# Kernel tuning notes

Measured on AMD Instinct MI355X. Metric: run time of the kernel, lower is better.

## Reference

```python
import jax, jax.numpy as jnp
import numpy as np

EPS = 1e-9
# i = 7,6,...,-1 use exp_factor = -(4**i); i = -2 uses 0.0 (matches torch's reversed(range(-2,8)))
EXP_FACTORS = np.array([-(4.0 ** i) for i in range(7, -2, -1)] + [0.0], dtype=np.float32)


def setup_inputs() -> dict:
    key = jax.random.key(0)
    k1, k2 = jax.random.split(key)
    B, N, D = 16, 2048, 3
    preds = jax.random.normal(k1, (B, N, D), dtype=jnp.float32)
    labels = jax.random.normal(k2, (B, N, D), dtype=jnp.float32)
    return {"preds": preds, "labels": labels}


def _pairwise_dist(p1, p2):
    # ||p1||^2 + ||p2||^2 - 2 p1 . p2  -> [B, N, N]
    p1n = jnp.sum(p1 * p1, axis=-1)[..., :, None]
    p2n = jnp.sum(p2 * p2, axis=-1)[..., None, :]
    return p1n + p2n - 2.0 * jnp.einsum('bnd,bmd->bnm', p1, p2)


def _approx_match(pwdist):
    B, N, _ = pwdist.shape
    match0 = jnp.zeros_like(pwdist)
    cost0 = jnp.ones((B, 1, N), dtype=pwdist.dtype)      # per-target remaining capacity
    curr0 = jnp.ones((B, N, 1), dtype=pwdist.dtype)      # per-source remaining currency

    def step(carry, ef):
        match, cost, currency = carry
        bids = jnp.exp(ef * pwdist) * cost
        bids = bids * currency / (jnp.sum(bids, axis=1, keepdims=True) + EPS)
        bid_wt = jnp.minimum(cost / (jnp.sum(bids, axis=1, keepdims=True) + EPS), 1.0)
        bids = bids * bid_wt
        match = match + bids
        cost = jnp.maximum(cost - jnp.sum(bids, axis=1, keepdims=True), 0.0)
        currency = jnp.maximum(currency - jnp.sum(bids, axis=2, keepdims=True), 0.0)
        return (match, cost, currency), None

    (match, _, _), _ = jax.lax.scan(step, (match0, cost0, curr0), jnp.asarray(EXP_FACTORS))
    return match


def reference(preds, labels):
    pwdist = _pairwise_dist(preds, labels)
    match = _approx_match(pwdist)
    return jnp.sum(match * pwdist)
```

## Files before the change

kernel.cpp:

```cpp
#include <hip/hip_runtime.h>
#include <cstddef>

#define BB    16
#define NN    2048
#define BN    (BB * NN)
#define TPB   512
#define SPLIT 16
#define TILE  128
#define MC    2
#define CHUNK 1024
#define EPSF  1e-9f

typedef float f2 __attribute__((ext_vector_type(2)));

__device__ __forceinline__ float fast_exp2(float x) {
#if __has_builtin(__builtin_amdgcn_exp2f)
    return __builtin_amdgcn_exp2f(x);
#else
    return exp2f(x);
#endif
}

__global__ void prep(const float* __restrict__ preds, const float* __restrict__ labels,
                     float4* __restrict__ Prow, float4* __restrict__ Lcol) {
    int i = blockIdx.x * 256 + threadIdx.x;
    const float* p = preds + (size_t)i * 3;
    float x = p[0], y = p[1], z = p[2];
    Prow[i] = make_float4(x, y, z, x * x + y * y + z * z);
    const float* l = labels + (size_t)i * 3;
    float a = l[0], c = l[1], d = l[2];
    Lcol[i] = make_float4(a, c, d, a * a + c * c + d * d);
}

__global__ __launch_bounds__(TPB, 4) void passA(
    const float4* __restrict__ Prow, const float4* __restrict__ Lcol,
    const float* __restrict__ curprev, float* __restrict__ curout,
    const float* __restrict__ RSp, const float* __restrict__ RRp,
    float* __restrict__ RSz, float* __restrict__ RRz,
    float* __restrict__ S, float* __restrict__ T,
    float* __restrict__ out, float c1, int k)
{
    __shared__ float s_cu[TILE];
    const int blk = blockIdx.x;
    const int split = blk & (SPLIT - 1), mc = (blk >> 4) & 1, b = blk >> 5;
    const int t = threadIdx.x;
    const int base = b * NN;
    const int row0 = split * TILE;

    if (t < TILE) {
        int idx = base + row0 + t;
        float cu, contrib = 0.f;
        if (k == 0) cu = 1.f;
        else {
            float cup = curprev[idx], rs = RSp[idx], rr = RRp[idx];
            contrib = cup * rr;
            cu = fmaxf(cup * (1.f - rs), 0.f);
        }
        s_cu[t] = cu;
        if (mc == 0) {
            curout[idx] = cu;
            RSz[idx] = 0.f; RRz[idx] = 0.f;
        }
        if (k > 0 && mc == 0) {
#pragma unroll
            for (int o = 32; o > 0; o >>= 1) contrib += __shfl_down(contrib, o, 64);
            if ((t & 63) == 0) atomicAdd(out, contrib);
        }
    }

    const int m0 = mc * CHUNK + t;
    float4 L0 = Lcol[base + m0], L1 = Lcol[base + m0 + TPB];
    const float n2c1 = -2.f * c1;
    f2 gx = (f2){n2c1 * L0.x, n2c1 * L1.x};
    f2 gy = (f2){n2c1 * L0.y, n2c1 * L1.y};
    f2 gz = (f2){n2c1 * L0.z, n2c1 * L1.z};
    f2 am = (f2){c1 * L0.w, c1 * L1.w};
    f2 Sa = (f2){0.f, 0.f}, Ta = (f2){0.f, 0.f};
    __syncthreads();

    const float4* prow = Prow + base + row0;
#pragma unroll 4
    for (int j = 0; j < TILE; j++) {
        float4 P = prow[j];
        float cu = s_cu[j];
        f2 arg = P.x * gx + (P.y * gy + (P.z * gz + (am + c1 * P.w)));
        f2 e; e.x = fast_exp2(arg.x); e.y = fast_exp2(arg.y);
        Sa += e;
        Ta += e * cu;
    }
    int i0 = base + m0, i1 = base + m0 + TPB;
    atomicAdd(&S[i0], Sa.x); atomicAdd(&S[i1], Sa.y);
    atomicAdd(&T[i0], Ta.x); atomicAdd(&T[i1], Ta.y);
}

__global__ __launch_bounds__(TPB, 4) void passB(
    const float4* __restrict__ Prow, const float4* __restrict__ Lcol,
    const float* __restrict__ S, const float* __restrict__ T,
    const float* __restrict__ costprev, float* __restrict__ costout,
    float* __restrict__ Sz, float* __restrict__ Tz,
    float* __restrict__ RS, float* __restrict__ RR,
    float c1, float invc1, int k, int last)
{
    __shared__ float s_cc[TILE];
    const int blk = blockIdx.x;
    const int split = blk & (SPLIT - 1), nc = (blk >> 4) & 1, b = blk >> 5;
    const int t = threadIdx.x;
    const int base = b * NN;
    const int col0 = split * TILE;

    if (t < TILE) {
        int idx = base + col0 + t;
        float Sv = S[idx], Tv = T[idx];
        float cost = (k == 0) ? 1.f : costprev[idx];
        float D1 = fmaf(cost, Sv, EPSF);
        float S2 = cost * Tv / D1;
        float bw = fminf(cost / (S2 + EPSF), 1.f);
        s_cc[t] = cost * bw / D1;
        if (nc == 0) {
            costout[idx] = fmaxf(fmaf(-S2, bw, cost), 0.f);
            Sz[idx] = 0.f; Tz[idx] = 0.f;
        }
    }

    const int n0 = nc * CHUNK + t;
    float4 P0 = Prow[base + n0], P1 = Prow[base + n0 + TPB];
    const float fx = last ? 1.f : -2.f * c1;
    f2 hx = (f2){fx * P0.x, fx * P1.x};
    f2 hy = (f2){fx * P0.y, fx * P1.y};
    f2 hz = (f2){fx * P0.z, fx * P1.z};
    f2 hn = last ? (f2){P0.w, P1.w} : (f2){c1 * P0.w, c1 * P1.w};
    f2 RSa = (f2){0.f, 0.f}, RRa = (f2){0.f, 0.f};
    __syncthreads();

    const float4* lcol = Lcol + base + col0;
    int i0 = base + n0, i1 = base + n0 + TPB;
    if (!last) {
#pragma unroll 4
        for (int j = 0; j < TILE; j++) {
            float4 L = lcol[j];
            float ccj = s_cc[j];
            f2 arg = L.x * hx + (L.y * hy + (L.z * hz + (hn + c1 * L.w)));
            f2 e; e.x = fast_exp2(arg.x); e.y = fast_exp2(arg.y);
            f2 w = e * ccj;
            RSa += w;
            RRa += w * arg;
        }
        atomicAdd(&RS[i0], RSa.x); atomicAdd(&RS[i1], RSa.y);
        atomicAdd(&RR[i0], RRa.x * invc1); atomicAdd(&RR[i1], RRa.y * invc1);
    } else {
#pragma unroll 4
        for (int j = 0; j < TILE; j++) {
            float4 L = lcol[j];
            float ccj = s_cc[j];
            f2 dot = L.x * hx + (L.y * hy + L.z * hz);
            f2 pw = (hn + L.w) - 2.f * dot;
            RRa += ccj * pw;
        }
        atomicAdd(&RR[i0], RRa.x); atomicAdd(&RR[i1], RRa.y);
    }
}

__global__ __launch_bounds__(TPB) void finalK(const float* __restrict__ cur,
                                              const float* __restrict__ RR,
                                              float* __restrict__ out)
{
    int i = blockIdx.x * TPB + threadIdx.x;
    float cb = cur[i] * RR[i];
#pragma unroll
    for (int o = 32; o > 0; o >>= 1) cb += __shfl_down(cb, o, 64);
    if ((threadIdx.x & 63) == 0) atomicAdd(out, cb);
}

extern "C" void kernel_launch(void* const* d_in, const int* in_sizes, int n_in,
                              void* d_out, int out_size, void* d_ws, size_t ws_size,
                              hipStream_t stream) {
    const float* preds  = (const float*)d_in[0];
    const float* labels = (const float*)d_in[1];
    float* out = (float*)d_out;
    float* ws  = (float*)d_ws;

    float* S[2]     = {ws + 0 * BN, ws + 2 * BN};
    float* T[2]     = {ws + 1 * BN, ws + 3 * BN};
    float* RS[2]    = {ws + 4 * BN, ws + 6 * BN};
    float* RR[2]    = {ws + 5 * BN, ws + 7 * BN};
    float* curb[2]  = {ws + 8 * BN, ws + 9 * BN};
    float* costb[2] = {ws + 10 * BN, ws + 11 * BN};
    float4* Prow = (float4*)(ws + 12 * BN);
    float4* Lcol = Prow + BN;

    hipMemsetAsync(d_out, 0, sizeof(float), stream);
    hipMemsetAsync(ws, 0, (size_t)2 * BN * sizeof(float), stream);
    prep<<<BN / 256, 256, 0, stream>>>(preds, labels, Prow, Lcol);

    static const float efs[10] = {-16384.0f, -4096.0f, -1024.0f, -256.0f, -64.0f,
                                  -16.0f, -4.0f, -1.0f, -0.25f, 0.0f};
    const float log2e = 1.44269504088896f;
    const int grid = BB * SPLIT * MC;
    for (int k = 0; k < 10; k++) {
        float c1 = efs[k] * log2e;
        float invc1 = (efs[k] != 0.0f) ? 1.0f / c1 : 0.0f;
        int pk = k & 1, pp = (k + 1) & 1;
        passA<<<grid, TPB, 0, stream>>>(Prow, Lcol,
            curb[pp], curb[pk],
            RS[pp], RR[pp],
            RS[pk], RR[pk],
            S[pk], T[pk],
            out, c1, k);
        passB<<<grid, TPB, 0, stream>>>(Prow, Lcol,
            S[pk], T[pk],
            costb[pk], costb[pp],
            S[pp], T[pp],
            RS[pk], RR[pk],
            c1, invc1, k, (k == 9) ? 1 : 0);
    }
    finalK<<<BN / TPB, TPB, 0, stream>>>(curb[1], RR[1], out);
}
```

Measured before the change: 376.7 us.

## Fuse all auction iterations into one persistent kernel with per-batch grid barriers

Replaces the 20 passA/passB launches plus finalK with a single persistent kernel of 256 blocks of 1024 threads. Consecutive phases are separated by spin-wait barriers that count arrivals per batch, and S/T/RS/RR are reset in place with system-scope atomics instead of double buffering. The exp-free last iteration (ef=0) is computed in closed form from per-batch reductions of cost-weighted label moments. This removes launch overhead and per-launch state reloads, at the cost of fewer blocks (less parallelism), spin-barrier latency, a risk of deadlock if not all blocks are co-resident, and staging tiles through global memory instead of LDS.

New measurement: 481.1 us. +27.7%, slower.

```diff
diff --git a/kernel.cpp b/kernel.cpp
--- a/kernel.cpp
+++ b/kernel.cpp
@@ -4,12 +4,13 @@
 #define BB    16
 #define NN    2048
 #define BN    (BB * NN)
-#define TPB   512
+#define TPB   1024
 #define SPLIT 16
 #define TILE  128
-#define MC    2
-#define CHUNK 1024
+#define GRIDB (BB * SPLIT)
 #define EPSF  1e-9f
+#define CTRPAD 64
+#define NBAR  20
 
 typedef float f2 __attribute__((ext_vector_type(2)));
 
@@ -19,6 +20,27 @@
 #else
     return exp2f(x);
 #endif
+}
+__device__ __forceinline__ float sysload(const float* p) {
+    return __hip_atomic_load(p, __ATOMIC_RELAXED, __HIP_MEMORY_SCOPE_SYSTEM);
+}
+__device__ __forceinline__ void sysstore(float* p, float v) {
+    __hip_atomic_store(p, v, __ATOMIC_RELAXED, __HIP_MEMORY_SCOPE_SYSTEM);
+}
+
+__device__ __forceinline__ void bbar(int* c) {
+    __syncthreads();
+    if (threadIdx.x == 0) {
+        __hip_atomic_fetch_add(c, 1, __ATOMIC_ACQ_REL, __HIP_MEMORY_SCOPE_SYSTEM);
+        int spins = 0;
+        while (__hip_atomic_load(c, __ATOMIC_RELAXED, __HIP_MEMORY_SCOPE_SYSTEM) < SPLIT) {
+#if __has_builtin(__builtin_amdgcn_s_sleep)
+            __builtin_amdgcn_s_sleep(8);
+#endif
+            if (++spins > (1 << 20)) break;
+        }
+    }
+    __syncthreads();
 }
 
 __global__ void prep(const float* __restrict__ preds, const float* __restrict__ labels,
@@ -32,143 +54,135 @@
     Lcol[i] = make_float4(a, c, d, a * a + c * c + d * d);
 }
 
-__global__ __launch_bounds__(TPB, 4) void passA(
+__global__ __launch_bounds__(TPB, 4) void emd_all(
     const float4* __restrict__ Prow, const float4* __restrict__ Lcol,
-    const float* __restrict__ curprev, float* __restrict__ curout,
-    const float* __restrict__ RSp, const float* __restrict__ RRp,
-    float* __restrict__ RSz, float* __restrict__ RRz,
     float* __restrict__ S, float* __restrict__ T,
-    float* __restrict__ out, float c1, int k)
+    float* __restrict__ RS, float* __restrict__ RR,
+    float* __restrict__ AUX, int* __restrict__ ctr,
+    float4* __restrict__ st4, float* __restrict__ st1,
+    float* __restrict__ out)
 {
-    __shared__ float s_cu[TILE];
-    const int blk = blockIdx.x;
-    const int split = blk & (SPLIT - 1), mc = (blk >> 4) & 1, b = blk >> 5;
+    __shared__ float s_red[2];
+    const int blk = blockIdx.x, split = blk & (SPLIT - 1), b = blk >> 4;
     const int t = threadIdx.x;
-    const int base = b * NN;
-    const int row0 = split * TILE;
-
-    if (t < TILE) {
-        int idx = base + row0 + t;
-        float cu, contrib = 0.f;
-        if (k == 0) cu = 1.f;
-        else {
-            float cup = curprev[idx], rs = RSp[idx], rr = RRp[idx];
-            contrib = cup * rr;
-            cu = fmaxf(cup * (1.f - rs), 0.f);
-        }
-        s_cu[t] = cu;
-        if (mc == 0) {
-            curout[idx] = cu;
-            RSz[idx] = 0.f; RRz[idx] = 0.f;
-        }
-        if (k > 0 && mc == 0) {
-#pragma unroll
-            for (int o = 32; o > 0; o >>= 1) contrib += __shfl_down(contrib, o, 64);
-            if ((t & 63) == 0) atomicAdd(out, contrib);
-        }
-    }
-
-    const int m0 = mc * CHUNK + t;
-    float4 L0 = Lcol[base + m0], L1 = Lcol[base + m0 + TPB];
-    const float n2c1 = -2.f * c1;
-    f2 gx = (f2){n2c1 * L0.x, n2c1 * L1.x};
-    f2 gy = (f2){n2c1 * L0.y, n2c1 * L1.y};
-    f2 gz = (f2){n2c1 * L0.z, n2c1 * L1.z};
-    f2 am = (f2){c1 * L0.w, c1 * L1.w};
-    f2 Sa = (f2){0.f, 0.f}, Ta = (f2){0.f, 0.f};
-    __syncthreads();
-
-    const float4* prow = Prow + base + row0;
-#pragma unroll 4
-    for (int j = 0; j < TILE; j++) {
-        float4 P = prow[j];
-        float cu = s_cu[j];
-        f2 arg = P.x * gx + (P.y * gy + (P.z * gz + (am + c1 * P.w)));
-        f2 e; e.x = fast_exp2(arg.x); e.y = fast_exp2(arg.y);
-        Sa += e;
-        Ta += e * cu;
-    }
-    int i0 = base + m0, i1 = base + m0 + TPB;
-    atomicAdd(&S[i0], Sa.x); atomicAdd(&S[i1], Sa.y);
-    atomicAdd(&T[i0], Ta.x); atomicAdd(&T[i1], Ta.y);
-}
-
-__global__ __launch_bounds__(TPB, 4) void passB(
-    const float4* __restrict__ Prow, const float4* __restrict__ Lcol,
-    const float* __restrict__ S, const float* __restrict__ T,
-    const float* __restrict__ costprev, float* __restrict__ costout,
-    float* __restrict__ Sz, float* __restrict__ Tz,
-    float* __restrict__ RS, float* __restrict__ RR,
-    float c1, float invc1, int k, int last)
-{
-    __shared__ float s_cc[TILE];
-    const int blk = blockIdx.x;
-    const int split = blk & (SPLIT - 1), nc = (blk >> 4) & 1, b = blk >> 5;
-    const int t = threadIdx.x;
-    const int base = b * NN;
-    const int col0 = split * TILE;
-
-    if (t < TILE) {
-        int idx = base + col0 + t;
-        float Sv = S[idx], Tv = T[idx];
-        float cost = (k == 0) ? 1.f : costprev[idx];
-        float D1 = fmaf(cost, Sv, EPSF);
-        float S2 = cost * Tv / D1;
-        float bw = fminf(cost / (S2 + EPSF), 1.f);
-        s_cc[t] = cost * bw / D1;
-        if (nc == 0) {
-            costout[idx] = fmaxf(fmaf(-S2, bw, cost), 0.f);
-            Sz[idx] = 0.f; Tz[idx] = 0.f;
-        }
-    }
-
-    const int n0 = nc * CHUNK + t;
-    float4 P0 = Prow[base + n0], P1 = Prow[base + n0 + TPB];
-    const float fx = last ? 1.f : -2.f * c1;
-    f2 hx = (f2){fx * P0.x, fx * P1.x};
-    f2 hy = (f2){fx * P0.y, fx * P1.y};
-    f2 hz = (f2){fx * P0.z, fx * P1.z};
-    f2 hn = last ? (f2){P0.w, P1.w} : (f2){c1 * P0.w, c1 * P1.w};
-    f2 RSa = (f2){0.f, 0.f}, RRa = (f2){0.f, 0.f};
-    __syncthreads();
-
-    const float4* lcol = Lcol + base + col0;
-    int i0 = base + n0, i1 = base + n0 + TPB;
-    if (!last) {
+    const int base = b * NN, i0 = base + split * TILE;
+    const int sb = blk * TILE;
+
+    float4 L0 = Lcol[base + t], L1 = Lcol[base + t + TPB];
+    float4 P0 = Prow[base + t], P1 = Prow[base + t + TPB];
+    float4 Pr = make_float4(0, 0, 0, 0), Lc = make_float4(0, 0, 0, 0);
+    float cur = 1.f, cost = 1.f, outacc = 0.f;
+    if (t < TILE) { Pr = Prow[i0 + t]; Lc = Lcol[i0 + t]; }
+
+    const float LOG2E = 1.44269504088896f;
+    int bar = 0;
+    for (int k = 0; k < 9; k++) {
+        const float ef = (k < 8) ? -(float)(1 << (14 - 2 * k)) : -0.25f;
+        const float c1 = ef * LOG2E, invc1 = 1.f / c1, n2 = -2.f * c1;
+
+        if (t < TILE) {
+            int idx = i0 + t;
+            if (k > 0) {
+                float rs = sysload(RS + idx), rr = sysload(RR + idx);
+                sysstore(RS + idx, 0.f); sysstore(RR + idx, 0.f);
+                outacc += cur * rr;
+                cur = fmaxf(cur * (1.f - rs), 0.f);
+            }
+            st4[sb + t] = make_float4(Pr.x, Pr.y, Pr.z, c1 * Pr.w);
+            st1[sb + t] = cur;
+        }
+        f2 gx = {n2 * L0.x, n2 * L1.x}, gy = {n2 * L0.y, n2 * L1.y};
+        f2 gz = {n2 * L0.z, n2 * L1.z}, am = {c1 * L0.w, c1 * L1.w};
+        f2 Sa = {0.f, 0.f}, Ta = {0.f, 0.f};
+        __syncthreads();
 #pragma unroll 4
         for (int j = 0; j < TILE; j++) {
-            float4 L = lcol[j];
-            float ccj = s_cc[j];
-            f2 arg = L.x * hx + (L.y * hy + (L.z * hz + (hn + c1 * L.w)));
+            float4 q = st4[sb + j];
+            float cu = st1[sb + j];
+            f2 arg = q.x * gx + (q.y * gy + (q.z * gz + (am + q.w)));
+            f2 e; e.x = fast_exp2(arg.x); e.y = fast_exp2(arg.y);
+            Sa += e;
+            Ta += e * cu;
+        }
+        atomicAdd(S + base + t, Sa.x); atomicAdd(S + base + t + TPB, Sa.y);
+        atomicAdd(T + base + t, Ta.x); atomicAdd(T + base + t + TPB, Ta.y);
+        bbar(ctr + (size_t)(bar * BB + b) * CTRPAD); bar++;
+
+        if (t < TILE) {
+            int idx = i0 + t;
+            float Sv = sysload(S + idx), Tv = sysload(T + idx);
+            sysstore(S + idx, 0.f); sysstore(T + idx, 0.f);
+            float D1 = fmaf(cost, Sv, EPSF);
+            float S2 = cost * Tv / D1;
+            float bw = fminf(cost / (S2 + EPSF), 1.f);
+            float cc = cost * bw / D1;
+            cost = fmaxf(fmaf(-S2, bw, cost), 0.f);
+            st4[sb + t] = make_float4(Lc.x, Lc.y, Lc.z, c1 * Lc.w);
+            st1[sb + t] = cc;
+        }
+        f2 hx = {n2 * P0.x, n2 * P1.x}, hy = {n2 * P0.y, n2 * P1.y};
+        f2 hz = {n2 * P0.z, n2 * P1.z}, hn = {c1 * P0.w, c1 * P1.w};
+        f2 RSa = {0.f, 0.f}, RRa = {0.f, 0.f};
+        __syncthreads();
+#pragma unroll 4
+        for (int j = 0; j < TILE; j++) {
+            float4 q = st4[sb + j];
+            float ccj = st1[sb + j];
+            f2 arg = q.x * hx + (q.y * hy + (q.z * hz + (hn + q.w)));
             f2 e; e.x = fast_exp2(arg.x); e.y = fast_exp2(arg.y);
             f2 w = e * ccj;
             RSa += w;
             RRa += w * arg;
         }
-        atomicAdd(&RS[i0], RSa.x); atomicAdd(&RS[i1], RSa.y);
-        atomicAdd(&RR[i0], RRa.x * invc1); atomicAdd(&RR[i1], RRa.y * invc1);
-    } else {
-#pragma unroll 4
-        for (int j = 0; j < TILE; j++) {
-            float4 L = lcol[j];
-            float ccj = s_cc[j];
-            f2 dot = L.x * hx + (L.y * hy + L.z * hz);
-            f2 pw = (hn + L.w) - 2.f * dot;
-            RRa += ccj * pw;
-        }
-        atomicAdd(&RR[i0], RRa.x); atomicAdd(&RR[i1], RRa.y);
-    }
-}
-
-__global__ __launch_bounds__(TPB) void finalK(const float* __restrict__ cur,
-                                              const float* __restrict__ RR,
-                                              float* __restrict__ out)
-{
-    int i = blockIdx.x * TPB + threadIdx.x;
-    float cb = cur[i] * RR[i];
+        atomicAdd(RS + base + t, RSa.x); atomicAdd(RS + base + t + TPB, RSa.y);
+        atomicAdd(RR + base + t, RRa.x * invc1);
+        atomicAdd(RR + base + t + TPB, RRa.y * invc1);
+        bbar(ctr + (size_t)(bar * BB + b) * CTRPAD); bar++;
+    }
+
+    if (t < TILE) {
+        int idx = i0 + t;
+        float rs = sysload(RS + idx), rr = sysload(RR + idx);
+        outacc += cur * rr;
+        cur = fmaxf(cur * (1.f - rs), 0.f);
+        float s = cur;
 #pragma unroll
-    for (int o = 32; o > 0; o >>= 1) cb += __shfl_down(cb, o, 64);
-    if ((threadIdx.x & 63) == 0) atomicAdd(out, cb);
+        for (int o = 32; o > 0; o >>= 1) s += __shfl_down(s, o, 64);
+        if ((t & 63) == 0) atomicAdd(AUX + b * 8 + 0, s);
+    }
+    bbar(ctr + (size_t)(bar * BB + b) * CTRPAD); bar++;
+    if (t < TILE) {
+        float T9 = sysload(AUX + b * 8 + 0);
+        float D1 = fmaf(cost, (float)NN, EPSF);
+        float S2 = cost * T9 / D1;
+        float bw = fminf(cost / (S2 + EPSF), 1.f);
+        float cc9 = cost * bw / D1;
+        float a0 = cc9, a1 = cc9 * Lc.w, a2 = cc9 * Lc.x, a3 = cc9 * Lc.y, a4 = cc9 * Lc.z;
+#pragma unroll
+        for (int o = 32; o > 0; o >>= 1) {
+            a0 += __shfl_down(a0, o, 64); a1 += __shfl_down(a1, o, 64);
+            a2 += __shfl_down(a2, o, 64); a3 += __shfl_down(a3, o, 64);
+            a4 += __shfl_down(a4, o, 64);
+        }
+        if ((t & 63) == 0) {
+            atomicAdd(AUX + b * 8 + 1, a0); atomicAdd(AUX + b * 8 + 2, a1);
+            atomicAdd(AUX + b * 8 + 3, a2); atomicAdd(AUX + b * 8 + 4, a3);
+            atomicAdd(AUX + b * 8 + 5, a4);
+        }
+    }
+    bbar(ctr + (size_t)(bar * BB + b) * CTRPAD); bar++;
+    if (t < TILE) {
+        float A = sysload(AUX + b * 8 + 1), Bv = sysload(AUX + b * 8 + 2);
+        float Cx = sysload(AUX + b * 8 + 3), Cy = sysload(AUX + b * 8 + 4);
+        float Cz = sysload(AUX + b * 8 + 5);
+        float rr9 = fmaf(A, Pr.w, Bv) - 2.f * (Pr.x * Cx + Pr.y * Cy + Pr.z * Cz);
+        outacc += cur * rr9;
+#pragma unroll
+        for (int o = 32; o > 0; o >>= 1) outacc += __shfl_down(outacc, o, 64);
+        if ((t & 63) == 0) s_red[t >> 6] = outacc;
+    }
+    __syncthreads();
+    if (t == 0) atomicAdd(out, s_red[0] + s_red[1]);
 }
 
 extern "C" void kernel_launch(void* const* d_in, const int* in_sizes, int n_in,
@@ -179,39 +193,21 @@
     float* out = (float*)d_out;
     float* ws  = (float*)d_ws;
 
-    float* S[2]     = {ws + 0 * BN, ws + 2 * BN};
-    float* T[2]     = {ws + 1 * BN, ws + 3 * BN};
-    float* RS[2]    = {ws + 4 * BN, ws + 6 * BN};
-    float* RR[2]    = {ws + 5 * BN, ws + 7 * BN};
-    float* curb[2]  = {ws + 8 * BN, ws + 9 * BN};
-    float* costb[2] = {ws + 10 * BN, ws + 11 * BN};
-    float4* Prow = (float4*)(ws + 12 * BN);
+    float* S   = ws;
+    float* T   = ws + BN;
+    float* RS  = ws + 2 * BN;
+    float* RR  = ws + 3 * BN;
+    float* AUX = ws + 4 * BN;
+    int*   ctr = (int*)(ws + 4 * BN + BB * 8);
+    size_t zfloats = 4 * (size_t)BN + BB * 8 + (size_t)NBAR * BB * CTRPAD;
+    float4* Prow = (float4*)(ws + zfloats);
     float4* Lcol = Prow + BN;
+    float4* st4  = Lcol + BN;
+    float*  st1  = (float*)(st4 + (size_t)GRIDB * TILE);
 
     hipMemsetAsync(d_out, 0, sizeof(float), stream);
-    hipMemsetAsync(ws, 0, (size_t)2 * BN * sizeof(float), stream);
+    hipMemsetAsync(ws, 0, zfloats * sizeof(float), stream);
     prep<<<BN / 256, 256, 0, stream>>>(preds, labels, Prow, Lcol);
-
-    static const float efs[10] = {-16384.0f, -4096.0f, -1024.0f, -256.0f, -64.0f,
-                                  -16.0f, -4.0f, -1.0f, -0.25f, 0.0f};
-    const float log2e = 1.44269504088896f;
-    const int grid = BB * SPLIT * MC;
-    for (int k = 0; k < 10; k++) {
-        float c1 = efs[k] * log2e;
-        float invc1 = (efs[k] != 0.0f) ? 1.0f / c1 : 0.0f;
-        int pk = k & 1, pp = (k + 1) & 1;
-        passA<<<grid, TPB, 0, stream>>>(Prow, Lcol,
-            curb[pp], curb[pk],
-            RS[pp], RR[pp],
-            RS[pk], RR[pk],
-            S[pk], T[pk],
-            out, c1, k);
-        passB<<<grid, TPB, 0, stream>>>(Prow, Lcol,
-            S[pk], T[pk],
-            costb[pk], costb[pp],
-            S[pp], T[pp],
-            RS[pk], RR[pk],
-            c1, invc1, k, (k == 9) ? 1 : 0);
-    }
-    finalK<<<BN / TPB, TPB, 0, stream>>>(curb[1], RR[1], out);
-}
+    emd_all<<<GRIDB, TPB, 0, stream>>>(Prow, Lcol, S, T, RS, RR, AUX, ctr,
+                                       st4, st1, out);
+}
```
